# Optimization experiments

Hardware: AMD Instinct MI355X
Metric: run time of the kernel (lower is better)

## Reference

```python
import jax, jax.numpy as jnp
import numpy as np

H = 200  # hidden size


def _init(k, shape):
    bound = 1.0 / np.sqrt(H)
    return jax.random.uniform(k, shape, jnp.float32, -bound, bound)


def setup_inputs() -> dict:
    key = jax.random.key(0)
    ks = jax.random.split(key, 11)
    T, B, D = 784, 512, 1
    x = jax.random.normal(ks[0], (T, 1, B, D), jnp.float32)
    return {
        "x": x,
        "W_in": _init(ks[1], (H, D)),
        "b_in": _init(ks[2], (H,)),
        # PyTorch LSTM gate order: i, f, g, o. b = b_ih + b_hh folded together.
        "Wih_f": _init(ks[3], (4 * H, H)),
        "Whh_f": _init(ks[4], (4 * H, H)),
        "b_f": _init(ks[5], (4 * H,)),
        "Wih_b": _init(ks[6], (4 * H, H)),
        "Whh_b": _init(ks[7], (4 * H, H)),
        "b_b": _init(ks[8], (4 * H,)),
        "W_fc": _init(ks[9], (10, 2 * H)),
        "b_fc": _init(ks[10], (10,)),
    }


def _lstm_dir(gates_in, Whh, reverse):
    # gates_in: (T, B, 4H) = x @ Wih.T + b, precomputed outside the scan.
    B = gates_in.shape[1]
    h0 = jnp.zeros((B, H), gates_in.dtype)

    def step(carry, g_in):
        h, c = carry
        g = g_in + h @ Whh.T  # (B, 4H)
        i, f, gg, o = jnp.split(g, 4, axis=-1)
        c = jax.nn.sigmoid(f) * c + jax.nn.sigmoid(i) * jnp.tanh(gg)
        h = jax.nn.sigmoid(o) * jnp.tanh(c)
        return (h, c), h

    _, hs = jax.lax.scan(step, (h0, h0), gates_in, reverse=reverse)
    return hs  # (T, B, H)


def reference(x, W_in, b_in, Wih_f, Whh_f, b_f, Wih_b, Whh_b, b_b, W_fc, b_fc):
    x = jnp.squeeze(x, 1)            # (T, B, D)
    x = x @ W_in.T + b_in            # (T, B, H)  input projection
    gf = x @ Wih_f.T + b_f           # (T, B, 4H) precomputed input gates, fwd dir
    gb = x @ Wih_b.T + b_b           # (T, B, 4H) precomputed input gates, bwd dir
    hf = _lstm_dir(gf, Whh_f, reverse=False)
    hb = _lstm_dir(gb, Whh_b, reverse=True)
    h = jnp.concatenate([hf, hb], axis=-1)  # (T, B, 2H)
    out = h @ W_fc.T + b_fc                 # (T, B, 10)
    return out.mean(axis=1)                 # (T, 10) -- matches x.mean(1)
```

## Files before the change

### kernel.cpp

```cpp
#include <hip/hip_runtime.h>


typedef short short8 __attribute__((ext_vector_type(8)));
typedef float f32x4 __attribute__((ext_vector_type(4)));
typedef unsigned short ushort_t;

#define T_STEPS 784
#define BATCH   512
#define HID     200
#define NKT     7
#define NMT     50
#define THREADS 512
#define HBUF    3584
#define NLDST   18
#define DYN_LDS (2 * HBUF * 2 + NLDST * NKT * 512 * 2)

#define WS_HPART 0
#define WS_UV    (40140800)
#define WS_WSW   (40140800 + 12800)

#define ACLOB \
  "a0","a1","a2","a3","a4","a5","a6","a7","a8","a9","a10","a11","a12","a13", \
  "a14","a15","a16","a17","a18","a19","a20","a21","a22","a23","a24","a25",   \
  "a26","a27","a28","a29","a30","a31","a32","a33","a34","a35","a36","a37",   \
  "a38","a39","a40","a41","a42","a43","a44","a45","a46","a47","a48","a49",   \
  "a50","a51","a52","a53","a54","a55","a56","a57","a58","a59","a60","a61",   \
  "a62","a63","a64","a65","a66","a67","a68","a69","a70","a71","a72","a73",   \
  "a74","a75","a76","a77","a78","a79","a80","a81","a82","a83","a84","a85",   \
  "a86","a87","a88","a89","a90","a91","a92","a93","a94","a95","a96","a97",   \
  "a98","a99","a100","a101","a102","a103","a104","a105","a106","a107",       \
  "a108","a109","a110","a111"

#define L1E 1.44269504088896340736f

__device__ __forceinline__ ushort_t f2bf(float f) {
  union { float f; unsigned u; } x; x.f = f;
  return (ushort_t)((x.u + 0x7FFFu + ((x.u >> 16) & 1u)) >> 16);
}
__device__ __forceinline__ float bf2f(ushort_t u) {
  union { unsigned u; float f; } x; x.u = (unsigned)u << 16; return x.f;
}

__device__ __forceinline__ float row16_sum(float v) {
  union { float f; int i; } a, b;
  a.f = v;
  b.i = __builtin_amdgcn_update_dpp(0, a.i, 0x118, 0xF, 0xF, true); a.f += b.f;
  b.i = __builtin_amdgcn_update_dpp(0, a.i, 0x114, 0xF, 0xF, true); a.f += b.f;
  b.i = __builtin_amdgcn_update_dpp(0, a.i, 0x112, 0xF, 0xF, true); a.f += b.f;
  b.i = __builtin_amdgcn_update_dpp(0, a.i, 0x111, 0xF, 0xF, true); a.f += b.f;
  return a.f;
}

#define PIN1(T, K, N0, N1, N2, N3)                                            \
  {                                                                           \
    union { short8 s; unsigned u[4]; } cv;                                    \
    cv.s = *(const short8*)(wg +                                              \
        ((size_t)((rbase + (T)) * NKT + (K))) * 512 + lane * 8);              \
    asm volatile("v_accvgpr_write_b32 a" #N0 ", %0\n\t"                       \
                 "v_accvgpr_write_b32 a" #N1 ", %1\n\t"                       \
                 "v_accvgpr_write_b32 a" #N2 ", %2\n\t"                       \
                 "v_accvgpr_write_b32 a" #N3 ", %3"                           \
                 :: "v"(cv.u[0]), "v"(cv.u[1]), "v"(cv.u[2]), "v"(cv.u[3])    \
                 : "a" #N0, "a" #N1, "a" #N2, "a" #N3);                       \
  }

__global__ void prep_uv(const float* __restrict__ Wih_f, const float* __restrict__ b_f,
                        const float* __restrict__ Wih_b, const float* __restrict__ b_b,
                        const float* __restrict__ W_in, const float* __restrict__ b_in,
                        float* __restrict__ uv_g) {
  const int dir = blockIdx.x, j = threadIdx.x;
  if (j >= HID) return;
  const float* Wih = dir ? Wih_b : Wih_f;
  const float* b   = dir ? b_b   : b_f;
  for (int q = 0; q < 4; ++q) {
    const int row = q * HID + j;
    const float* wr = Wih + (size_t)row * HID;
    float u = 0.f, v = 0.f;
    for (int k = 0; k < HID; ++k) {
      u = fmaf(wr[k], W_in[k], u);
      v = fmaf(wr[k], b_in[k], v);
    }
    uv_g[(size_t)dir * 1600 + j * 8 + q]     = u;
    uv_g[(size_t)dir * 1600 + j * 8 + 4 + q] = v + b[row];
  }
}

__global__ void prep_w(const float* __restrict__ Whh_f, const float* __restrict__ Whh_b,
                       const float* __restrict__ uv_g, ushort_t* __restrict__ w_sw) {
  const int bid = blockIdx.x, lane = threadIdx.x;
  const int dir = bid / (NMT * NKT);
  const int rem = bid % (NMT * NKT);
  const int mt = rem / NKT, kt = rem % NKT;
  const float* W = dir ? Whh_b : Whh_f;
  const int m = lane & 15;
  const int q = m & 3;
  const int j = mt * 4 + (m >> 2);
  const int row = q * HID + j;
  const int grp = lane >> 4;
  const float sq = (q == 2) ? (-2.f * L1E) : (-L1E);
  short8 v8 = {0, 0, 0, 0, 0, 0, 0, 0};
  if (kt < 6) {
#pragma unroll
    for (int e = 0; e < 8; ++e)
      v8[e] = (short)f2bf(sq * W[(size_t)row * HID + kt * 32 + grp * 8 + e]);
  } else if (grp == 0) {
#pragma unroll
    for (int e = 0; e < 8; ++e)
      v8[e] = (short)f2bf(sq * W[(size_t)row * HID + 192 + e]);
  } else if (grp == 1) {
    const float U = sq * uv_g[(size_t)dir * 1600 + j * 8 + q];
    const float V = sq * uv_g[(size_t)dir * 1600 + j * 8 + 4 + q];
    const ushort_t vhi = f2bf(V), uhi = f2bf(U);
    v8[0] = (short)vhi;
    v8[1] = (short)f2bf(V - bf2f(vhi));
    v8[2] = (short)uhi;
    v8[3] = (short)f2bf(U - bf2f(uhi));
    v8[4] = (short)uhi;
  }
  *(short8*)(w_sw + (size_t)bid * 512 + (size_t)lane * 8) = v8;
}

__device__ __forceinline__ void cell_update(const f32x4 a, const int haddr,
                                            ushort_t* __restrict__ hnext,
                                            float& c, float& hold) {
  const float ei = __builtin_amdgcn_exp2f(a[0]);
  const float ef = __builtin_amdgcn_exp2f(a[1]);
  const float eg = __builtin_amdgcn_exp2f(a[2]);
  const float eo = __builtin_amdgcn_exp2f(a[3]);
  const float pi = 1.f + ei, pf = 1.f + ef, pg = 1.f + eg;
  const float pig = pi * pg;
  const float R1 = __builtin_amdgcn_rcpf(pig * pf);
  const float sf = pig * R1;
  const float sitg = (1.f - eg) * pf * R1;
  const float cn = fmaf(sf, c, sitg);
  c = cn;
  const float ec = __builtin_amdgcn_exp2f(fminf(-2.f * L1E * cn, 83.f));
  const float R2 = __builtin_amdgcn_rcpf((1.f + ec) * (1.f + eo));
  const float h = (1.f - ec) * R2;
  unsigned hu;
  asm("v_cvt_pk_bf16_f32 %0, %1, %2" : "=v"(hu) : "v"(h), "v"(0.f));
  hnext[haddr] = (ushort_t)hu;
  hold = row16_sum(h);
}

template <int NLDS>
__device__ __forceinline__ void scan_loop(
    const int rbase, const int lfirst, const int dir, const int b0,
    const int lane, const int wv, const int blk, const ushort_t* __restrict__ wg,
    const float* __restrict__ x, float* __restrict__ hpart,
    ushort_t* __restrict__ h_lds, const ushort_t* __restrict__ w_lds_my) {
  constexpr int NREG = 4;
  constexpr int NT = NREG + NLDS;
  const int bcol = lane & 15, krow = lane >> 4;
  const bool xw = (wv == 0) & (krow == 1);

  PIN1(0, 0,  0,  1,  2,  3)  PIN1(0, 1,  4,  5,  6,  7)
  PIN1(0, 2,  8,  9, 10, 11)  PIN1(0, 3, 12, 13, 14, 15)
  PIN1(0, 4, 16, 17, 18, 19)  PIN1(0, 5, 20, 21, 22, 23)
  PIN1(0, 6, 24, 25, 26, 27)
  PIN1(1, 0, 28, 29, 30, 31)  PIN1(1, 1, 32, 33, 34, 35)
  PIN1(1, 2, 36, 37, 38, 39)  PIN1(1, 3, 40, 41, 42, 43)
  PIN1(1, 4, 44, 45, 46, 47)  PIN1(1, 5, 48, 49, 50, 51)
  PIN1(1, 6, 52, 53, 54, 55)
  PIN1(2, 0, 56, 57, 58, 59)  PIN1(2, 1, 60, 61, 62, 63)
  PIN1(2, 2, 64, 65, 66, 67)  PIN1(2, 3, 68, 69, 70, 71)
  PIN1(2, 4, 72, 73, 74, 75)  PIN1(2, 5, 76, 77, 78, 79)
  PIN1(2, 6, 80, 81, 82, 83)
  PIN1(3, 0, 84, 85, 86, 87)  PIN1(3, 1, 88, 89, 90, 91)
  PIN1(3, 2, 92, 93, 94, 95)  PIN1(3, 3, 96, 97, 98, 99)
  PIN1(3, 4, 100, 101, 102, 103)  PIN1(3, 5, 104, 105, 106, 107)
  PIN1(3, 6, 108, 109, 110, 111)
  asm volatile("s_nop 7\n\ts_nop 7");

  f32x4 zero4 = {0.f, 0.f, 0.f, 0.f};
  asm volatile("" : "+v"(zero4));

  int haddr[NT];
#pragma unroll
  for (int i = 0; i < NT; ++i) {
    const int tile = (i < NREG) ? rbase + i : lfirst + (i - NREG);
    const int j = tile * 4 + krow;
    haddr[i] = (j >> 5) * 512 + (bcol | (((j >> 3) & 3) << 4)) * 8 + (j & 7);
  }
  float c[NT], hold[NT];
#pragma unroll
  for (int i = 0; i < NT; ++i) { c[i] = 0.f; hold[i] = 0.f; }

  const int jb = rbase * 4 + krow;
  const int jl = lfirst * 4 + krow;
  int t_prev = 0, cur = 0;

  for (int s = 0; s < T_STEPS; ++s) {
    const int t = dir ? (T_STEPS - 1 - s) : s;

    short8 bf[NKT];
#pragma unroll
    for (int kt = 0; kt < NKT; ++kt)
      bf[kt] = *(const short8*)&h_lds[cur * HBUF + kt * 512 + lane * 8];

    const int sn = (s + 1 < T_STEPS) ? s + 1 : s;
    float xn = 0.f;
    if (xw) xn = x[(size_t)(dir ? T_STEPS - 1 - sn : sn) * BATCH + b0 + bcol];

    if (s > 0 && bcol == 15) {
      float* hp = hpart + ((size_t)t_prev * 64 + blk) * 200;
#pragma unroll
      for (int i = 0; i < NREG; ++i) hp[jb + 4 * i] = hold[i];
#pragma unroll
      for (int i = 0; i < NLDS; ++i) hp[jl + 4 * i] = hold[NREG + i];
    }

    ushort_t* hnext = h_lds + (cur ^ 1) * HBUF;

    f32x4 a0, a1, a2, a3;
    asm volatile(
      "s_nop 1\n\t"
      "v_mfma_f32_16x16x32_bf16 %0, a[0:3],    %4, %11\n\t"
      "v_mfma_f32_16x16x32_bf16 %1, a[28:31],  %4, %11\n\t"
      "v_mfma_f32_16x16x32_bf16 %2, a[56:59],  %4, %11\n\t"
      "v_mfma_f32_16x16x32_bf16 %3, a[84:87],  %4, %11\n\t"
      "v_mfma_f32_16x16x32_bf16 %0, a[4:7],    %5, %0\n\t"
      "v_mfma_f32_16x16x32_bf16 %1, a[32:35],  %5, %1\n\t"
      "v_mfma_f32_16x16x32_bf16 %2, a[60:63],  %5, %2\n\t"
      "v_mfma_f32_16x16x32_bf16 %3, a[88:91],  %5, %3\n\t"
      "v_mfma_f32_16x16x32_bf16 %0, a[8:11],   %6, %0\n\t"
      "v_mfma_f32_16x16x32_bf16 %1, a[36:39],  %6, %1\n\t"
      "v_mfma_f32_16x16x32_bf16 %2, a[64:67],  %6, %2\n\t"
      "v_mfma_f32_16x16x32_bf16 %3, a[92:95],  %6, %3\n\t"
      "v_mfma_f32_16x16x32_bf16 %0, a[12:15],  %7, %0\n\t"
      "v_mfma_f32_16x16x32_bf16 %1, a[40:43],  %7, %1\n\t"
      "v_mfma_f32_16x16x32_bf16 %2, a[68:71],  %7, %2\n\t"
      "v_mfma_f32_16x16x32_bf16 %3, a[96:99],  %7, %3\n\t"
      "v_mfma_f32_16x16x32_bf16 %0, a[16:19],  %8, %0\n\t"
      "v_mfma_f32_16x16x32_bf16 %1, a[44:47],  %8, %1\n\t"
      "v_mfma_f32_16x16x32_bf16 %2, a[72:75],  %8, %2\n\t"
      "v_mfma_f32_16x16x32_bf16 %3, a[100:103],%8, %3\n\t"
      "v_mfma_f32_16x16x32_bf16 %0, a[20:23],  %9, %0\n\t"
      "v_mfma_f32_16x16x32_bf16 %1, a[48:51],  %9, %1\n\t"
      "v_mfma_f32_16x16x32_bf16 %2, a[76:79],  %9, %2\n\t"
      "v_mfma_f32_16x16x32_bf16 %3, a[104:107],%9, %3\n\t"
      "v_mfma_f32_16x16x32_bf16 %0, a[24:27],  %10, %0\n\t"
      "v_mfma_f32_16x16x32_bf16 %1, a[52:55],  %10, %1\n\t"
      "v_mfma_f32_16x16x32_bf16 %2, a[80:83],  %10, %2\n\t"
      "v_mfma_f32_16x16x32_bf16 %3, a[108:111],%10, %3\n\t"
      "s_nop 7\n\ts_nop 7"
      : "=&v"(a0), "=&v"(a1), "=&v"(a2), "=&v"(a3)
      : "v"(bf[0]), "v"(bf[1]), "v"(bf[2]), "v"(bf[3]), "v"(bf[4]),
        "v"(bf[5]), "v"(bf[6]), "v"(zero4)
      : ACLOB);

    f32x4 bl[NLDS];
    if constexpr (NLDS == 2) {
      {
        const short8 af0 = *(const short8*)&w_lds_my[(0 * NKT + 0) * 512 + lane * 8];
        const short8 af1 = *(const short8*)&w_lds_my[(1 * NKT + 0) * 512 + lane * 8];
        asm volatile("s_nop 1\n\t"
                     "v_mfma_f32_16x16x32_bf16 %0, %2, %4, %5\n\t"
                     "v_mfma_f32_16x16x32_bf16 %1, %3, %4, %5"
                     : "=&v"(bl[0]), "=&v"(bl[1])
                     : "v"(af0), "v"(af1), "v"(bf[0]), "v"(zero4));
      }
#pragma unroll
      for (int kt = 1; kt < NKT - 1; ++kt) {
        const short8 af0 = *(const short8*)&w_lds_my[(0 * NKT + kt) * 512 + lane * 8];
        const short8 af1 = *(const short8*)&w_lds_my[(1 * NKT + kt) * 512 + lane * 8];
        asm volatile("v_mfma_f32_16x16x32_bf16 %0, %2, %4, %0\n\t"
                     "v_mfma_f32_16x16x32_bf16 %1, %3, %4, %1"
                     : "+v"(bl[0]), "+v"(bl[1])
                     : "v"(af0), "v"(af1), "v"(bf[kt]));
      }
      {
        const short8 af0 = *(const short8*)&w_lds_my[(0 * NKT + 6) * 512 + lane * 8];
        const short8 af1 = *(const short8*)&w_lds_my[(1 * NKT + 6) * 512 + lane * 8];
        asm volatile("v_mfma_f32_16x16x32_bf16 %0, %2, %4, %0\n\t"
                     "v_mfma_f32_16x16x32_bf16 %1, %3, %4, %1\n\t"
                     "s_nop 7\n\ts_nop 7"
                     : "+v"(bl[0]), "+v"(bl[1])
                     : "v"(af0), "v"(af1), "v"(bf[6]));
      }
    } else {
      {
        const short8 af0 = *(const short8*)&w_lds_my[(0 * NKT + 0) * 512 + lane * 8];
        const short8 af1 = *(const short8*)&w_lds_my[(1 * NKT + 0) * 512 + lane * 8];
        const short8 af2 = *(const short8*)&w_lds_my[(2 * NKT + 0) * 512 + lane * 8];
        asm volatile("s_nop 1\n\t"
                     "v_mfma_f32_16x16x32_bf16 %0, %3, %6, %7\n\t"
                     "v_mfma_f32_16x16x32_bf16 %1, %4, %6, %7\n\t"
                     "v_mfma_f32_16x16x32_bf16 %2, %5, %6, %7"
                     : "=&v"(bl[0]), "=&v"(bl[1]), "=&v"(bl[2])
                     : "v"(af0), "v"(af1), "v"(af2), "v"(bf[0]), "v"(zero4));
      }
#pragma unroll
      for (int kt = 1; kt < NKT - 1; ++kt) {
        const short8 af0 = *(const short8*)&w_lds_my[(0 * NKT + kt) * 512 + lane * 8];
        const short8 af1 = *(const short8*)&w_lds_my[(1 * NKT + kt) * 512 + lane * 8];
        const short8 af2 = *(const short8*)&w_lds_my[(2 * NKT + kt) * 512 + lane * 8];
        asm volatile("v_mfma_f32_16x16x32_bf16 %0, %3, %6, %0\n\t"
                     "v_mfma_f32_16x16x32_bf16 %1, %4, %6, %1\n\t"
                     "v_mfma_f32_16x16x32_bf16 %2, %5, %6, %2"
                     : "+v"(bl[0]), "+v"(bl[1]), "+v"(bl[2])
                     : "v"(af0), "v"(af1), "v"(af2), "v"(bf[kt]));
      }
      {
        const short8 af0 = *(const short8*)&w_lds_my[(0 * NKT + 6) * 512 + lane * 8];
        const short8 af1 = *(const short8*)&w_lds_my[(1 * NKT + 6) * 512 + lane * 8];
        const short8 af2 = *(const short8*)&w_lds_my[(2 * NKT + 6) * 512 + lane * 8];
        asm volatile("v_mfma_f32_16x16x32_bf16 %0, %3, %6, %0\n\t"
                     "v_mfma_f32_16x16x32_bf16 %1, %4, %6, %1\n\t"
                     "v_mfma_f32_16x16x32_bf16 %2, %5, %6, %2\n\t"
                     "s_nop 7\n\ts_nop 7"
                     : "+v"(bl[0]), "+v"(bl[1]), "+v"(bl[2])
                     : "v"(af0), "v"(af1), "v"(af2), "v"(bf[6]));
      }
    }

    ushort_t* hn = hnext;
    cell_update(a0, haddr[0], hn, c[0], hold[0]);
    cell_update(a1, haddr[1], hn, c[1], hold[1]);
    cell_update(a2, haddr[2], hn, c[2], hold[2]);
    cell_update(a3, haddr[3], hn, c[3], hold[3]);
#pragma unroll
    for (int i = 0; i < NLDS; ++i)
      cell_update(bl[i], haddr[NREG + i], hn, c[NREG + i], hold[NREG + i]);

    if (xw) {
      const ushort_t hi = f2bf(xn);
      const ushort_t lo = f2bf(xn - bf2f(hi));
      const int sb = 6 * 512 + lane * 8;
      hnext[sb + 2] = hi;
      hnext[sb + 3] = hi;
      hnext[sb + 4] = lo;
    }

    t_prev = t;
    asm volatile("s_waitcnt lgkmcnt(0)\n\ts_barrier" ::: "memory");
    cur ^= 1;
  }
  if (bcol == 15) {
    float* hp = hpart + ((size_t)t_prev * 64 + blk) * 200;
#pragma unroll
    for (int i = 0; i < NREG; ++i) hp[jb + 4 * i] = hold[i];
#pragma unroll
    for (int i = 0; i < NLDS; ++i) hp[jl + 4 * i] = hold[NREG + i];
  }
}

__global__ __launch_bounds__(THREADS, 2) void lstm_main(
    const float* __restrict__ x, const ushort_t* __restrict__ w_sw,
    float* __restrict__ hpart) {
  extern __shared__ __align__(16) ushort_t dynlds[];
  ushort_t* h_lds = dynlds;
  ushort_t* w_lds = dynlds + 2 * HBUF;

  const int tid = threadIdx.x;
  const int lane = tid & 63;
  const int wv = tid >> 6;
  const int blk = blockIdx.x;
  const int dir = blk & 1;
  const int b0 = (blk >> 1) * 16;

  const ushort_t* wg = w_sw + (size_t)dir * NMT * NKT * 512;

  for (int i = tid; i < HBUF; i += THREADS) ((unsigned*)h_lds)[i] = 0;
  for (int i = tid; i < NLDST * NKT * 64; i += THREADS)
    *(short8*)&w_lds[(size_t)i * 8] =
        *(const short8*)(wg + (size_t)32 * NKT * 512 + (size_t)i * 8);
  __syncthreads();

  if (tid < 16) {
    const int t0 = dir ? T_STEPS - 1 : 0;
    const float x0 = x[(size_t)t0 * BATCH + b0 + tid];
    const ushort_t hi = f2bf(x0);
    const ushort_t lo = f2bf(x0 - bf2f(hi));
    const int sb = 6 * 512 + (16 + tid) * 8;
    h_lds[sb + 0] = 0x3F80; h_lds[sb + 1] = 0x3F80;
    h_lds[HBUF + sb + 0] = 0x3F80; h_lds[HBUF + sb + 1] = 0x3F80;
    h_lds[sb + 2] = hi; h_lds[sb + 3] = hi; h_lds[sb + 4] = lo;
  }
  __syncthreads();

  const int rbase = 4 * wv;
  const int lfirst = (wv < 6) ? (32 + 2 * wv) : (44 + 3 * (wv - 6));
  const ushort_t* wl = w_lds + (size_t)(lfirst - 32) * NKT * 512;
  if (wv < 6)
    scan_loop<2>(rbase, lfirst, dir, b0, lane, wv, blk, wg, x, hpart, h_lds, wl);
  else
    scan_loop<3>(rbase, lfirst, dir, b0, lane, wv, blk, wg, x, hpart, h_lds, wl);
}

__global__ void out_proj(const float* __restrict__ hpart, const float* __restrict__ Wfc,
                         const float* __restrict__ bfc, float* __restrict__ out) {
  const int t = blockIdx.x, tid = threadIdx.x;
  const float* hb = hpart + (size_t)t * 64 * 200;
  float a[10] = {0.f, 0.f, 0.f, 0.f, 0.f, 0.f, 0.f, 0.f, 0.f, 0.f};
  for (int col = tid; col < 400; col += 256) {
    const int dir = (col >= HID) ? 1 : 0;
    const int j = col - dir * HID;
    float s = 0.f;
#pragma unroll
    for (int sl = 0; sl < 32; ++sl) s += hb[(size_t)((sl << 1) | dir) * 200 + j];
    const float hv = s * (1.f / 512.f);
#pragma unroll
    for (int o = 0; o < 10; ++o) a[o] = fmaf(hv, Wfc[o * 400 + col], a[o]);
  }
#pragma unroll
  for (int o = 0; o < 10; ++o) {
    float v = a[o];
    for (int m = 32; m; m >>= 1) v += __shfl_xor(v, m);
    a[o] = v;
  }
  __shared__ float red[4][10];
  if ((tid & 63) == 0)
#pragma unroll
    for (int o = 0; o < 10; ++o) red[tid >> 6][o] = a[o];
  __syncthreads();
  if (tid < 10)
    out[t * 10 + tid] = bfc[tid] + red[0][tid] + red[1][tid] + red[2][tid] + red[3][tid];
}

extern "C" void kernel_launch(void* const* d_in, const int* in_sizes, int n_in,
                              void* d_out, int out_size, void* d_ws, size_t ws_size,
                              hipStream_t stream) {
  const float* x     = (const float*)d_in[0];
  const float* W_in  = (const float*)d_in[1];
  const float* b_in  = (const float*)d_in[2];
  const float* Wih_f = (const float*)d_in[3];
  const float* Whh_f = (const float*)d_in[4];
  const float* b_f   = (const float*)d_in[5];
  const float* Wih_b = (const float*)d_in[6];
  const float* Whh_b = (const float*)d_in[7];
  const float* b_b   = (const float*)d_in[8];
  const float* W_fc  = (const float*)d_in[9];
  const float* b_fc  = (const float*)d_in[10];
  float* out = (float*)d_out;

  char* ws = (char*)d_ws;
  float*    hpart = (float*)(ws + WS_HPART);
  float*    uv_g  = (float*)(ws + WS_UV);
  ushort_t* w_sw  = (ushort_t*)(ws + WS_WSW);

  hipFuncSetAttribute((const void*)lstm_main,
                      hipFuncAttributeMaxDynamicSharedMemorySize, DYN_LDS);

  prep_uv<<<2, 256, 0, stream>>>(Wih_f, b_f, Wih_b, b_b, W_in, b_in, uv_g);
  prep_w<<<2 * NMT * NKT, 64, 0, stream>>>(Whh_f, Whh_b, uv_g, w_sw);
  lstm_main<<<64, THREADS, DYN_LDS, stream>>>(x, w_sw, hpart);
  out_proj<<<T_STEPS, 256, 0, stream>>>(hpart, W_fc, b_fc, out);
}
```

Baseline: 1.407 ms.

## Spread LSTM recurrent tiles over twelve waves instead of eight

Raises the block from 8 to 12 waves so each wave owns 3 register-pinned weight tiles plus 1–2 LDS-resident tiles, instead of 4 pinned plus 2–3 LDS tiles. This shortens the serial MFMA chain and cell-update work per wave on each timestep of the sequential scan, and shrinks the LDS weight region from 18 to 14 tiles. In exchange, barrier synchronisation covers more waves and the launch-bound occupancy hint changes from 2 to 3.

```diff
diff --git a/kernel.cpp b/kernel.cpp
--- a/kernel.cpp
+++ b/kernel.cpp
@@ -10,9 +10,9 @@
 #define HID     200
 #define NKT     7
 #define NMT     50
-#define THREADS 512
+#define THREADS 768
 #define HBUF    3584
-#define NLDST   18
+#define NLDST   14
 #define DYN_LDS (2 * HBUF * 2 + NLDST * NKT * 512 * 2)
 
 #define WS_HPART 0
@@ -26,10 +26,7 @@
   "a38","a39","a40","a41","a42","a43","a44","a45","a46","a47","a48","a49",   \
   "a50","a51","a52","a53","a54","a55","a56","a57","a58","a59","a60","a61",   \
   "a62","a63","a64","a65","a66","a67","a68","a69","a70","a71","a72","a73",   \
-  "a74","a75","a76","a77","a78","a79","a80","a81","a82","a83","a84","a85",   \
-  "a86","a87","a88","a89","a90","a91","a92","a93","a94","a95","a96","a97",   \
-  "a98","a99","a100","a101","a102","a103","a104","a105","a106","a107",       \
-  "a108","a109","a110","a111"
+  "a74","a75","a76","a77","a78","a79","a80","a81","a82","a83"
 
 #define L1E 1.44269504088896340736f
 
@@ -149,7 +146,7 @@
     const int lane, const int wv, const int blk, const ushort_t* __restrict__ wg,
     const float* __restrict__ x, float* __restrict__ hpart,
     ushort_t* __restrict__ h_lds, const ushort_t* __restrict__ w_lds_my) {
-  constexpr int NREG = 4;
+  constexpr int NREG = 3;
   constexpr int NT = NREG + NLDS;
   const int bcol = lane & 15, krow = lane >> 4;
   const bool xw = (wv == 0) & (krow == 1);
@@ -166,10 +163,6 @@
   PIN1(2, 2, 64, 65, 66, 67)  PIN1(2, 3, 68, 69, 70, 71)
   PIN1(2, 4, 72, 73, 74, 75)  PIN1(2, 5, 76, 77, 78, 79)
   PIN1(2, 6, 80, 81, 82, 83)
-  PIN1(3, 0, 84, 85, 86, 87)  PIN1(3, 1, 88, 89, 90, 91)
-  PIN1(3, 2, 92, 93, 94, 95)  PIN1(3, 3, 96, 97, 98, 99)
-  PIN1(3, 4, 100, 101, 102, 103)  PIN1(3, 5, 104, 105, 106, 107)
-  PIN1(3, 6, 108, 109, 110, 111)
   asm volatile("s_nop 7\n\ts_nop 7");
 
   f32x4 zero4 = {0.f, 0.f, 0.f, 0.f};
@@ -212,45 +205,57 @@
 
     ushort_t* hnext = h_lds + (cur ^ 1) * HBUF;
 
-    f32x4 a0, a1, a2, a3;
+    f32x4 a0, a1, a2;
     asm volatile(
       "s_nop 1\n\t"
-      "v_mfma_f32_16x16x32_bf16 %0, a[0:3],    %4, %11\n\t"
-      "v_mfma_f32_16x16x32_bf16 %1, a[28:31],  %4, %11\n\t"
-      "v_mfma_f32_16x16x32_bf16 %2, a[56:59],  %4, %11\n\t"
-      "v_mfma_f32_16x16x32_bf16 %3, a[84:87],  %4, %11\n\t"
-      "v_mfma_f32_16x16x32_bf16 %0, a[4:7],    %5, %0\n\t"
-      "v_mfma_f32_16x16x32_bf16 %1, a[32:35],  %5, %1\n\t"
-      "v_mfma_f32_16x16x32_bf16 %2, a[60:63],  %5, %2\n\t"
-      "v_mfma_f32_16x16x32_bf16 %3, a[88:91],  %5, %3\n\t"
-      "v_mfma_f32_16x16x32_bf16 %0, a[8:11],   %6, %0\n\t"
-      "v_mfma_f32_16x16x32_bf16 %1, a[36:39],  %6, %1\n\t"
-      "v_mfma_f32_16x16x32_bf16 %2, a[64:67],  %6, %2\n\t"
-      "v_mfma_f32_16x16x32_bf16 %3, a[92:95],  %6, %3\n\t"
-      "v_mfma_f32_16x16x32_bf16 %0, a[12:15],  %7, %0\n\t"
-      "v_mfma_f32_16x16x32_bf16 %1, a[40:43],  %7, %1\n\t"
-      "v_mfma_f32_16x16x32_bf16 %2, a[68:71],  %7, %2\n\t"
-      "v_mfma_f32_16x16x32_bf16 %3, a[96:99],  %7, %3\n\t"
-      "v_mfma_f32_16x16x32_bf16 %0, a[16:19],  %8, %0\n\t"
-      "v_mfma_f32_16x16x32_bf16 %1, a[44:47],  %8, %1\n\t"
-      "v_mfma_f32_16x16x32_bf16 %2, a[72:75],  %8, %2\n\t"
-      "v_mfma_f32_16x16x32_bf16 %3, a[100:103],%8, %3\n\t"
-      "v_mfma_f32_16x16x32_bf16 %0, a[20:23],  %9, %0\n\t"
-      "v_mfma_f32_16x16x32_bf16 %1, a[48:51],  %9, %1\n\t"
-      "v_mfma_f32_16x16x32_bf16 %2, a[76:79],  %9, %2\n\t"
-      "v_mfma_f32_16x16x32_bf16 %3, a[104:107],%9, %3\n\t"
-      "v_mfma_f32_16x16x32_bf16 %0, a[24:27],  %10, %0\n\t"
-      "v_mfma_f32_16x16x32_bf16 %1, a[52:55],  %10, %1\n\t"
-      "v_mfma_f32_16x16x32_bf16 %2, a[80:83],  %10, %2\n\t"
-      "v_mfma_f32_16x16x32_bf16 %3, a[108:111],%10, %3\n\t"
+      "v_mfma_f32_16x16x32_bf16 %0, a[0:3],    %3, %10\n\t"
+      "v_mfma_f32_16x16x32_bf16 %1, a[28:31],  %3, %10\n\t"
+      "v_mfma_f32_16x16x32_bf16 %2, a[56:59],  %3, %10\n\t"
+      "v_mfma_f32_16x16x32_bf16 %0, a[4:7],    %4, %0\n\t"
+      "v_mfma_f32_16x16x32_bf16 %1, a[32:35],  %4, %1\n\t"
+      "v_mfma_f32_16x16x32_bf16 %2, a[60:63],  %4, %2\n\t"
+      "v_mfma_f32_16x16x32_bf16 %0, a[8:11],   %5, %0\n\t"
+      "v_mfma_f32_16x16x32_bf16 %1, a[36:39],  %5, %1\n\t"
+      "v_mfma_f32_16x16x32_bf16 %2, a[64:67],  %5, %2\n\t"
+      "v_mfma_f32_16x16x32_bf16 %0, a[12:15],  %6, %0\n\t"
+      "v_mfma_f32_16x16x32_bf16 %1, a[40:43],  %6, %1\n\t"
+      "v_mfma_f32_16x16x32_bf16 %2, a[68:71],  %6, %2\n\t"
+      "v_mfma_f32_16x16x32_bf16 %0, a[16:19],  %7, %0\n\t"
+      "v_mfma_f32_16x16x32_bf16 %1, a[44:47],  %7, %1\n\t"
+      "v_mfma_f32_16x16x32_bf16 %2, a[72:75],  %7, %2\n\t"
+      "v_mfma_f32_16x16x32_bf16 %0, a[20:23],  %8, %0\n\t"
+      "v_mfma_f32_16x16x32_bf16 %1, a[48:51],  %8, %1\n\t"
+      "v_mfma_f32_16x16x32_bf16 %2, a[76:79],  %8, %2\n\t"
+      "v_mfma_f32_16x16x32_bf16 %0, a[24:27],  %9, %0\n\t"
+      "v_mfma_f32_16x16x32_bf16 %1, a[52:55],  %9, %1\n\t"
+      "v_mfma_f32_16x16x32_bf16 %2, a[80:83],  %9, %2\n\t"
       "s_nop 7\n\ts_nop 7"
-      : "=&v"(a0), "=&v"(a1), "=&v"(a2), "=&v"(a3)
+      : "=&v"(a0), "=&v"(a1), "=&v"(a2)
       : "v"(bf[0]), "v"(bf[1]), "v"(bf[2]), "v"(bf[3]), "v"(bf[4]),
         "v"(bf[5]), "v"(bf[6]), "v"(zero4)
       : ACLOB);
 
     f32x4 bl[NLDS];
-    if constexpr (NLDS == 2) {
+    if constexpr (NLDS == 1) {
+      {
+        const short8 af = *(const short8*)&w_lds_my[0 * 512 + lane * 8];
+        asm volatile("s_nop 1\n\t"
+                     "v_mfma_f32_16x16x32_bf16 %0, %1, %2, %3"
+                     : "=&v"(bl[0]) : "v"(af), "v"(bf[0]), "v"(zero4));
+      }
+#pragma unroll
+      for (int kt = 1; kt < NKT - 1; ++kt) {
+        const short8 af = *(const short8*)&w_lds_my[kt * 512 + lane * 8];
+        asm volatile("v_mfma_f32_16x16x32_bf16 %0, %1, %2, %0"
+                     : "+v"(bl[0]) : "v"(af), "v"(bf[kt]));
+      }
+      {
+        const short8 af = *(const short8*)&w_lds_my[6 * 512 + lane * 8];
+        asm volatile("v_mfma_f32_16x16x32_bf16 %0, %1, %2, %0\n\t"
+                     "s_nop 7\n\ts_nop 7"
+                     : "+v"(bl[0]) : "v"(af), "v"(bf[6]));
+      }
+    } else {
       {
         const short8 af0 = *(const short8*)&w_lds_my[(0 * NKT + 0) * 512 + lane * 8];
         const short8 af1 = *(const short8*)&w_lds_my[(1 * NKT + 0) * 512 + lane * 8];
@@ -278,50 +283,14 @@
                      : "+v"(bl[0]), "+v"(bl[1])
                      : "v"(af0), "v"(af1), "v"(bf[6]));
       }
-    } else {
-      {
-        const short8 af0 = *(const short8*)&w_lds_my[(0 * NKT + 0) * 512 + lane * 8];
-        const short8 af1 = *(const short8*)&w_lds_my[(1 * NKT + 0) * 512 + lane * 8];
-        const short8 af2 = *(const short8*)&w_lds_my[(2 * NKT + 0) * 512 + lane * 8];
-        asm volatile("s_nop 1\n\t"
-                     "v_mfma_f32_16x16x32_bf16 %0, %3, %6, %7\n\t"
-                     "v_mfma_f32_16x16x32_bf16 %1, %4, %6, %7\n\t"
-                     "v_mfma_f32_16x16x32_bf16 %2, %5, %6, %7"
-                     : "=&v"(bl[0]), "=&v"(bl[1]), "=&v"(bl[2])
-                     : "v"(af0), "v"(af1), "v"(af2), "v"(bf[0]), "v"(zero4));
-      }
-#pragma unroll
-      for (int kt = 1; kt < NKT - 1; ++kt) {
-        const short8 af0 = *(const short8*)&w_lds_my[(0 * NKT + kt) * 512 + lane * 8];
-        const short8 af1 = *(const short8*)&w_lds_my[(1 * NKT + kt) * 512 + lane * 8];
-        const short8 af2 = *(const short8*)&w_lds_my[(2 * NKT + kt) * 512 + lane * 8];
-        asm volatile("v_mfma_f32_16x16x32_bf16 %0, %3, %6, %0\n\t"
-                     "v_mfma_f32_16x16x32_bf16 %1, %4, %6, %1\n\t"
-                     "v_mfma_f32_16x16x32_bf16 %2, %5, %6, %2"
-                     : "+v"(bl[0]), "+v"(bl[1]), "+v"(bl[2])
-                     : "v"(af0), "v"(af1), "v"(af2), "v"(bf[kt]));
-      }
-      {
-        const short8 af0 = *(const short8*)&w_lds_my[(0 * NKT + 6) * 512 + lane * 8];
-        const short8 af1 = *(const short8*)&w_lds_my[(1 * NKT + 6) * 512 + lane * 8];
-        const short8 af2 = *(const short8*)&w_lds_my[(2 * NKT + 6) * 512 + lane * 8];
-        asm volatile("v_mfma_f32_16x16x32_bf16 %0, %3, %6, %0\n\t"
-                     "v_mfma_f32_16x16x32_bf16 %1, %4, %6, %1\n\t"
-                     "v_mfma_f32_16x16x32_bf16 %2, %5, %6, %2\n\t"
-                     "s_nop 7\n\ts_nop 7"
-                     : "+v"(bl[0]), "+v"(bl[1]), "+v"(bl[2])
-                     : "v"(af0), "v"(af1), "v"(af2), "v"(bf[6]));
-      }
     }
 
-    ushort_t* hn = hnext;
-    cell_update(a0, haddr[0], hn, c[0], hold[0]);
-    cell_update(a1, haddr[1], hn, c[1], hold[1]);
-    cell_update(a2, haddr[2], hn, c[2], hold[2]);
-    cell_update(a3, haddr[3], hn, c[3], hold[3]);
+    cell_update(a0, haddr[0], hnext, c[0], hold[0]);
+    cell_update(a1, haddr[1], hnext, c[1], hold[1]);
+    cell_update(a2, haddr[2], hnext, c[2], hold[2]);
 #pragma unroll
     for (int i = 0; i < NLDS; ++i)
-      cell_update(bl[i], haddr[NREG + i], hn, c[NREG + i], hold[NREG + i]);
+      cell_update(bl[i], haddr[NREG + i], hnext, c[NREG + i], hold[NREG + i]);
 
     if (xw) {
       const ushort_t hi = f2bf(xn);
@@ -345,7 +314,7 @@
   }
 }
 
-__global__ __launch_bounds__(THREADS, 2) void lstm_main(
+__global__ __launch_bounds__(THREADS, 3) void lstm_main(
     const float* __restrict__ x, const ushort_t* __restrict__ w_sw,
     float* __restrict__ hpart) {
   extern __shared__ __align__(16) ushort_t dynlds[];
@@ -364,7 +333,7 @@
   for (int i = tid; i < HBUF; i += THREADS) ((unsigned*)h_lds)[i] = 0;
   for (int i = tid; i < NLDST * NKT * 64; i += THREADS)
     *(short8*)&w_lds[(size_t)i * 8] =
-        *(const short8*)(wg + (size_t)32 * NKT * 512 + (size_t)i * 8);
+        *(const short8*)(wg + (size_t)36 * NKT * 512 + (size_t)i * 8);
   __syncthreads();
 
   if (tid < 16) {
@@ -379,13 +348,17 @@
   }
   __syncthreads();
 
-  const int rbase = 4 * wv;
-  const int lfirst = (wv < 6) ? (32 + 2 * wv) : (44 + 3 * (wv - 6));
-  const ushort_t* wl = w_lds + (size_t)(lfirst - 32) * NKT * 512;
-  if (wv < 6)
-    scan_loop<2>(rbase, lfirst, dir, b0, lane, wv, blk, wg, x, hpart, h_lds, wl);
-  else
-    scan_loop<3>(rbase, lfirst, dir, b0, lane, wv, blk, wg, x, hpart, h_lds, wl);
+  const int rbase = 3 * wv;
+  if (wv < 10) {
+    scan_loop<1>(rbase, 36 + wv, dir, b0, lane, wv, blk, wg, x, hpart, h_lds,
+                 w_lds + (size_t)wv * NKT * 512);
+  } else if (wv == 10) {
+    scan_loop<2>(rbase, 46, dir, b0, lane, wv, blk, wg, x, hpart, h_lds,
+                 w_lds + (size_t)10 * NKT * 512);
+  } else {
+    scan_loop<2>(rbase, 48, dir, b0, lane, wv, blk, wg, x, hpart, h_lds,
+                 w_lds + (size_t)12 * NKT * 512);
+  }
 }
 
 __global__ void out_proj(const float* __restrict__ hpart, const float* __restrict__ Wfc,
```

New measurement: 1.938 ms. 1.38x slower.
